# Kernel optimization log

Measured on AMD Instinct MI355X. Metric: run time of the kernel, lower is better.

Reference implementation:

```python
import jax, jax.numpy as jnp
import numpy as np

H = 1024          # hidden_size
RH = 2 * H        # router/expert hidden (hidden_multiplier=2)
E = 3             # num_experts
B, T, P = 8, 2048, 64
LN_EPS = 1e-5


def _layer_norm(x, gamma, beta):
    mu = jnp.mean(x, axis=-1, keepdims=True)
    var = jnp.mean(jnp.square(x - mu), axis=-1, keepdims=True)
    return (x - mu) * jax.lax.rsqrt(var + LN_EPS) * gamma + beta


def setup_inputs() -> dict:
    key = jax.random.key(0)
    ks = jax.random.split(key, 24)
    s = lambda fan_in: 1.0 / np.sqrt(fan_in)
    inp = {
        "mix_hidden_states": jax.random.normal(ks[0], (B, T, H), jnp.float32),
        "global_anchor": jax.random.normal(ks[1], (B, H), jnp.float32),
        "prototype_bank": jax.random.normal(ks[2], (B, P, H), jnp.float32),
        # LayerNorm
        "ln_gamma": jnp.ones((H,), jnp.float32),
        "ln_beta": jnp.zeros((H,), jnp.float32),
        # retriever (no bias)
        "Wq": jax.random.normal(ks[3], (H, H), jnp.float32) * s(H),
        "Wk": jax.random.normal(ks[4], (H, H), jnp.float32) * s(H),
        "Wv": jax.random.normal(ks[5], (H, H), jnp.float32) * s(H),
        # router linear: 3H -> E
        "router_W": jax.random.normal(ks[6], (3 * H, E), jnp.float32) * s(3 * H),
        "router_b": jnp.zeros((E,), jnp.float32),
        # experts stacked: [E, 3H, RH] and [E, RH, H]
        "e_w1": jax.random.normal(ks[7], (E, 3 * H, RH), jnp.float32) * s(3 * H),
        "e_b1": jnp.zeros((E, RH), jnp.float32),
        "e_w2": jax.random.normal(ks[8], (E, RH, H), jnp.float32) * s(RH),
        "e_b2": jnp.zeros((E, H), jnp.float32),
        # gate MLP: 3H -> H -> H
        "gate_w1": jax.random.normal(ks[9], (3 * H, H), jnp.float32) * s(3 * H),
        "gate_b1": jnp.zeros((H,), jnp.float32),
        "gate_w2": jax.random.normal(ks[10], (H, H), jnp.float32) * s(H),
        "gate_b2": jnp.zeros((H,), jnp.float32),
        # out_proj (zero-init in torch, but use random for nontrivial baseline)
        "out_w": jax.random.normal(ks[11], (H, H), jnp.float32) * s(H),
        "out_b": jnp.zeros((H,), jnp.float32),
    }
    return inp


def reference(mix_hidden_states, global_anchor, prototype_bank,
              ln_gamma, ln_beta, Wq, Wk, Wv, router_W, router_b,
              e_w1, e_b1, e_w2, e_b2, gate_w1, gate_b1, gate_w2, gate_b2,
              out_w, out_b):
    x = mix_hidden_states
    nx = _layer_norm(x, ln_gamma, ln_beta)                      # [B,T,H]

    # --- evidence retriever (cross-attention over prototype bank) ---
    q = nx @ Wq                                                 # [B,T,H]
    k = prototype_bank @ Wk                                     # [B,P,H]
    v = prototype_bank @ Wv                                     # [B,P,H]
    scores = jnp.einsum('bth,bph->btp', q, k) * (H ** -0.5)
    weights = jax.nn.softmax(scores, axis=-1)
    evidence = jnp.einsum('btp,bph->bth', weights, v)           # [B,T,H]

    anchor = jnp.broadcast_to(global_anchor[:, None, :], nx.shape)
    combined = jnp.concatenate([nx, evidence, anchor], axis=-1) # [B,T,3H]

    # --- soft MoE router ---
    router_logits = combined @ router_W + router_b              # [B,T,E]
    router_probs = jax.nn.softmax(router_logits, axis=-1)
    h = jax.nn.silu(jnp.einsum('btc,ecr->bter', combined, e_w1) + e_b1)
    expert_out = jnp.einsum('bter,erh->bteh', h, e_w2) + e_b2   # [B,T,E,H]
    routed = jnp.sum(expert_out * router_probs[..., None], axis=-2)

    # --- sigmoid gate + residual ---
    g = jax.nn.sigmoid(jax.nn.silu(combined @ gate_w1 + gate_b1) @ gate_w2 + gate_b2)
    refined_delta = g * (routed @ out_w + out_b)
    return x + refined_delta
```

## Files before the change

### kernel.cpp

```cpp
#include <hip/hip_runtime.h>

typedef unsigned short u16;
typedef __bf16 bf16x8 __attribute__((ext_vector_type(8)));
typedef float f32x4 __attribute__((ext_vector_type(4)));

__device__ __forceinline__ float b2f(u16 u) {
  union { unsigned int i; float f; } x; x.i = ((unsigned int)u) << 16; return x.f;
}
__device__ __forceinline__ u16 f2b(float f) {
  union { float f; unsigned int i; } x; x.f = f;
  unsigned int r = (x.i + 0x7fffu + ((x.i >> 16) & 1u)) >> 16;
  return (u16)r;
}

__device__ __forceinline__ void async16(const void* g, void* l) {
  __builtin_amdgcn_global_load_lds((const __attribute__((address_space(1))) void*)g,
                                   (__attribute__((address_space(3))) void*)l, 16, 0, 0);
}

#define EPI_BF16    0
#define EPI_SILU    1
#define EPI_SIGMOID 2
#define EPI_ROUTED  3
#define EPI_FINAL   4
#define EPI_F32SC   5

__global__ __launch_bounds__(256) void gemm_bt(
    const u16* __restrict__ A, int lda, long long sA,
    const u16* __restrict__ B, int ldb, long long sB,
    const float* __restrict__ bias,
    const float* __restrict__ bcast, int ldbc,
    void* __restrict__ Cv, int ldc, long long sC,
    int M, int N, int K,
    int epi, float scale,
    const float* __restrict__ rowscale, int rs_off, int accum,
    const float* __restrict__ Xres, const u16* __restrict__ Gg)
{
  __shared__ u16 As[2][128 * 32];
  __shared__ u16 Bs[2][128 * 32];
  const int z = blockIdx.z;
  A += (long long)z * sA;
  B += (long long)z * sB;
  const int m0 = blockIdx.y * 128, n0 = blockIdx.x * 128;
  const int tid = threadIdx.x;
  const int lane = tid & 63, w = tid >> 6;
  const int wm = w >> 1, wn = w & 1;

  const int sr = lane >> 2;
  const int sc = (lane & 3) * 8;
  int ra0 = m0 + w * 16 + sr;      if (ra0 > M - 1) ra0 = M - 1;
  int ra1 = m0 + 64 + w * 16 + sr; if (ra1 > M - 1) ra1 = M - 1;
  int rb0 = n0 + w * 16 + sr;      if (rb0 > N - 1) rb0 = N - 1;
  int rb1 = n0 + 64 + w * 16 + sr; if (rb1 > N - 1) rb1 = N - 1;
  const u16* pa0 = A + (long long)ra0 * lda + sc;
  const u16* pa1 = A + (long long)ra1 * lda + sc;
  const u16* pb0 = B + (long long)rb0 * ldb + sc;
  const u16* pb1 = B + (long long)rb1 * ldb + sc;
  const int lw = w * 512;

  f32x4 acc[4][4] = {};

  const int kch = (lane >> 4) * 8;
  const int rr = lane & 15;

  async16(pa0, &As[0][lw]);
  async16(pa1, &As[0][2048 + lw]);
  async16(pb0, &Bs[0][lw]);
  async16(pb1, &Bs[0][2048 + lw]);

  int cur = 0;
  for (int k0 = 0; k0 < K; k0 += 32) {
    __syncthreads();
    const int kn = k0 + 32;
    if (kn < K) {
      const int nb = cur ^ 1;
      async16(pa0 + kn, &As[nb][lw]);
      async16(pa1 + kn, &As[nb][2048 + lw]);
      async16(pb0 + kn, &Bs[nb][lw]);
      async16(pb1 + kn, &Bs[nb][2048 + lw]);
    }
    bf16x8 af[4], bfr[4];
#pragma unroll
    for (int mi = 0; mi < 4; ++mi)
      af[mi] = *(const bf16x8*)(&As[cur][(wm * 64 + mi * 16 + rr) * 32 + kch]);
#pragma unroll
    for (int ni = 0; ni < 4; ++ni)
      bfr[ni] = *(const bf16x8*)(&Bs[cur][(wn * 64 + ni * 16 + rr) * 32 + kch]);
#pragma unroll
    for (int mi = 0; mi < 4; ++mi)
#pragma unroll
      for (int ni = 0; ni < 4; ++ni)
        acc[mi][ni] = __builtin_amdgcn_mfma_f32_16x16x32_bf16(af[mi], bfr[ni], acc[mi][ni], 0, 0, 0);
    cur ^= 1;
  }

  u16* Cb = (u16*)Cv;
  float* Cf = (float*)Cv;
#pragma unroll
  for (int ni = 0; ni < 4; ++ni) {
    int col = n0 + wn * 64 + ni * 16 + (lane & 15);
    if (col >= N) continue;
    float bv = bias ? bias[col] : 0.0f;
#pragma unroll
    for (int mi = 0; mi < 4; ++mi) {
#pragma unroll
      for (int r = 0; r < 4; ++r) {
        int row = m0 + wm * 64 + mi * 16 + (lane >> 4) * 4 + r;
        if (row >= M) continue;
        float v = acc[mi][ni][r] + bv;
        if (bcast) v += bcast[(row >> 11) * ldbc + col];
        long long cidx = (long long)z * sC + (long long)row * ldc + col;
        if (epi == EPI_BF16) {
          Cb[cidx] = f2b(v);
        } else if (epi == EPI_SILU) {
          Cb[cidx] = f2b(v / (1.0f + __expf(-v)));
        } else if (epi == EPI_SIGMOID) {
          Cb[cidx] = f2b(1.0f / (1.0f + __expf(-v)));
        } else if (epi == EPI_ROUTED) {
          float rs = rowscale[row * 3 + rs_off];
          if (accum) Cf[cidx] += rs * v; else Cf[cidx] = rs * v;
        } else if (epi == EPI_FINAL) {
          long long xi = (long long)row * ldc + col;
          Cf[cidx] = Xres[xi] + b2f(Gg[xi]) * v;
        } else {
          Cf[cidx] = v * scale;
        }
      }
    }
  }
}

#define CFENCE asm volatile("" ::: "memory")

#define STAGE(H, T_, SLOT) do { \
  const u16* s_ = ((H) & 1) ? srcB : srcA; \
  const long long ld_ = ((H) & 1) ? (long long)ldb : (long long)lda; \
  const u16* p_ = s_ + (((H) >> 1) ? 128 * ld_ : 0) + (long long)(T_) * 64; \
  u16* lb_ = &lds8[SLOT][w * 1024]; \
  async16(p_, lb_); \
  async16(p_ + 8 * ld_, lb_ + 512); \
} while (0)

#define READA(SLOT) do { \
  _Pragma("unroll") for (int fm = 0; fm < 4; ++fm) { \
    af[fm][0] = *(const bf16x8*)&lds8[SLOT][(wm * 64 + fm * 16 + rr) * 64 + cx0]; \
    af[fm][1] = *(const bf16x8*)&lds8[SLOT][(wm * 64 + fm * 16 + rr) * 64 + cx1]; \
  } } while (0)

#define READB(SLOT) do { \
  _Pragma("unroll") for (int fn = 0; fn < 2; ++fn) { \
    bf[fn][0] = *(const bf16x8*)&lds8[SLOT][(wn * 32 + fn * 16 + rr) * 64 + cx0]; \
    bf[fn][1] = *(const bf16x8*)&lds8[SLOT][(wn * 32 + fn * 16 + rr) * 64 + cx1]; \
  } } while (0)

#define MMAC(QM, QN) do { \
  __builtin_amdgcn_s_setprio(1); \
  _Pragma("unroll") for (int fm = 0; fm < 4; ++fm) { \
    _Pragma("unroll") for (int fn = 0; fn < 2; ++fn) { \
      acc[(QM)*4+fm][(QN)*2+fn] = __builtin_amdgcn_mfma_f32_16x16x32_bf16(af[fm][0], bf[fn][0], acc[(QM)*4+fm][(QN)*2+fn], 0, 0, 0); \
      acc[(QM)*4+fm][(QN)*2+fn] = __builtin_amdgcn_mfma_f32_16x16x32_bf16(af[fm][1], bf[fn][1], acc[(QM)*4+fm][(QN)*2+fn], 0, 0, 0); \
    } } \
  __builtin_amdgcn_s_setprio(0); \
} while (0)

__global__ __launch_bounds__(512, 2) void gemm256_bt(
    const u16* __restrict__ A, int lda,
    const u16* __restrict__ B, int ldb,
    const float* __restrict__ bias,
    const float* __restrict__ bcast, int ldbc,
    void* __restrict__ Cv, int ldc,
    int M, int N, int K,
    int epi, float scale,
    const float* __restrict__ rowscale, int rs_off, int accum,
    const float* __restrict__ Xres, const u16* __restrict__ Gg)
{
  __shared__ u16 lds8[8][8192];

  int gx = gridDim.x;
  int nwg = gx * gridDim.y;
  int bid = blockIdx.y * gx + blockIdx.x;
  int bx, by;
  if ((nwg & 7) == 0) {
    int cpx = nwg >> 3;
    int swz = (bid & 7) * cpx + (bid >> 3);
    bx = swz % gx; by = swz / gx;
  } else { bx = blockIdx.x; by = blockIdx.y; }
  const int m0 = by * 256, n0 = bx * 256;

  const int tid = threadIdx.x;
  const int lane = tid & 63, w = tid >> 6;
  const int wm = w >> 2, wn = w & 3;
  const int rr = lane & 15;

  const int cx0 = (((lane >> 4) * 16)      ^ ((lane & 7) << 4)) >> 1;
  const int cx1 = ((64 + (lane >> 4) * 16) ^ ((lane & 7) << 4)) >> 1;

  const int rloc = w * 16 + (lane >> 3);
  const int swz8 = 8 * ((lane & 7) ^ (lane >> 3));
  const u16* srcA = A + (long long)(m0 + rloc) * lda + swz8;
  const u16* srcB = B + (long long)(n0 + rloc) * ldb + swz8;

  f32x4 acc[8][4] = {};
  bf16x8 af[4][2], bf[2][2];

  const int T = K >> 6;

  STAGE(0, 0, 0); STAGE(1, 0, 1); STAGE(2, 0, 2); STAGE(3, 0, 3);
  if (T > 1) { STAGE(0, 1, 4); STAGE(1, 1, 5); }
  if (T > 1) { asm volatile("s_waitcnt vmcnt(4)" ::: "memory"); }
  else       { asm volatile("s_waitcnt vmcnt(0)" ::: "memory"); }
  __builtin_amdgcn_s_barrier();
  CFENCE;

  for (int s = 0; s < T; ++s) {
    const int par = (s & 1) * 4;
    const int opar = 4 - par;

    READA(par + 0);
    READB(par + 1);
    CFENCE;
    if (s + 1 < T) STAGE(2, s + 1, opar + 2);
    __builtin_amdgcn_s_barrier();
    CFENCE;
    MMAC(0, 0);
    __builtin_amdgcn_s_barrier();
    CFENCE;

    READB(par + 3);
    CFENCE;
    if (s + 1 < T) STAGE(3, s + 1, opar + 3);
    __builtin_amdgcn_s_barrier();
    CFENCE;
    MMAC(0, 1);
    __builtin_amdgcn_s_barrier();
    CFENCE;

    READA(par + 2);
    READB(par + 1);
    CFENCE;
    if (s + 2 < T) STAGE(0, s + 2, par + 0);
    __builtin_amdgcn_s_barrier();
    CFENCE;
    MMAC(1, 0);
    __builtin_amdgcn_s_barrier();
    CFENCE;

    READB(par + 3);
    CFENCE;
    if (s + 2 < T) {
      STAGE(1, s + 2, par + 1);
      asm volatile("s_waitcnt vmcnt(4)" ::: "memory");
    } else if (s + 1 < T) {
      asm volatile("s_waitcnt vmcnt(0)" ::: "memory");
    }
    __builtin_amdgcn_s_barrier();
    CFENCE;
    MMAC(1, 1);
    __builtin_amdgcn_s_barrier();
    CFENCE;
  }

  u16* Cb = (u16*)Cv;
  float* Cf = (float*)Cv;
#pragma unroll
  for (int ni = 0; ni < 4; ++ni) {
    int col = n0 + (ni >> 1) * 128 + wn * 32 + (ni & 1) * 16 + (lane & 15);
    float bv = bias ? bias[col] : 0.0f;
#pragma unroll
    for (int mi = 0; mi < 8; ++mi) {
#pragma unroll
      for (int r = 0; r < 4; ++r) {
        int row = m0 + (mi >> 2) * 128 + wm * 64 + (mi & 3) * 16 + (lane >> 4) * 4 + r;
        float v = acc[mi][ni][r] + bv;
        if (bcast) v += bcast[(row >> 11) * ldbc + col];
        long long cidx = (long long)row * ldc + col;
        if (epi == EPI_BF16) {
          Cb[cidx] = f2b(v);
        } else if (epi == EPI_SILU) {
          Cb[cidx] = f2b(v / (1.0f + __expf(-v)));
        } else if (epi == EPI_SIGMOID) {
          Cb[cidx] = f2b(1.0f / (1.0f + __expf(-v)));
        } else if (epi == EPI_ROUTED) {
          float rs = rowscale[row * 3 + rs_off];
          if (accum) Cf[cidx] += rs * v; else Cf[cidx] = rs * v;
        } else if (epi == EPI_FINAL) {
          long long xi = (long long)row * ldc + col;
          Cf[cidx] = Xres[xi] + b2f(Gg[xi]) * v;
        } else {
          Cf[cidx] = v * scale;
        }
      }
    }
  }
}

__global__ __launch_bounds__(256) void transpose_cvt(const float* __restrict__ in, u16* __restrict__ out, int R, int C) {
  __shared__ float tile[32][33];
  int c0 = blockIdx.x * 32, r0 = blockIdx.y * 32;
  int tx = threadIdx.x & 31, ty = threadIdx.x >> 5;
#pragma unroll
  for (int i = 0; i < 4; ++i) {
    int r = ty + i * 8;
    tile[r][tx] = in[(long long)(r0 + r) * C + c0 + tx];
  }
  __syncthreads();
#pragma unroll
  for (int i = 0; i < 4; ++i) {
    int r = ty + i * 8;
    out[(long long)(c0 + r) * R + r0 + tx] = f2b(tile[tx][r]);
  }
}

__global__ __launch_bounds__(256) void cvt_bf16(const float* __restrict__ in, u16* __restrict__ out, int n) {
  for (int i = blockIdx.x * 256 + threadIdx.x; i < n; i += gridDim.x * 256)
    out[i] = f2b(in[i]);
}

__global__ __launch_bounds__(256) void ln_kernel(const float* __restrict__ x, const float* __restrict__ gamma,
                                                 const float* __restrict__ beta, u16* __restrict__ ne) {
  int t = blockIdx.x;
  int tid = threadIdx.x;
  const float* xr = x + (long long)t * 1024;
  float v[4];
  float s = 0.f, sq = 0.f;
#pragma unroll
  for (int i = 0; i < 4; ++i) {
    v[i] = xr[tid * 4 + i];
    s += v[i]; sq += v[i] * v[i];
  }
#pragma unroll
  for (int d = 32; d; d >>= 1) { s += __shfl_xor(s, d, 64); sq += __shfl_xor(sq, d, 64); }
  __shared__ float ls[4], lq[4];
  int w = tid >> 6, lane = tid & 63;
  if (lane == 0) { ls[w] = s; lq[w] = sq; }
  __syncthreads();
  s = ls[0] + ls[1] + ls[2] + ls[3];
  sq = lq[0] + lq[1] + lq[2] + lq[3];
  float mean = s * (1.0f / 1024.0f);
  float var = sq * (1.0f / 1024.0f) - mean * mean;
  float rstd = rsqrtf(var + 1e-5f);
  long long base = (long long)t * 2048;
#pragma unroll
  for (int i = 0; i < 4; ++i) {
    int c = tid * 4 + i;
    ne[base + c] = f2b((v[i] - mean) * rstd * gamma[c] + beta[c]);
  }
}

#define ANCH_KC 32
__global__ __launch_bounds__(256) void anchor_partial(const float* __restrict__ anchor, const float* __restrict__ W,
                                                      int ldw, int N, float* __restrict__ partial) {
  int n = blockIdx.x * 256 + threadIdx.x;
  if (n >= N) return;
  const int kc = blockIdx.y;
  const int kper = 1024 / ANCH_KC;
  const int k0 = kc * kper;
  float acc[8] = {};
  for (int k = k0; k < k0 + kper; ++k) {
    float wv = W[(long long)(2048 + k) * ldw + n];
#pragma unroll
    for (int b = 0; b < 8; ++b) acc[b] += anchor[b * 1024 + k] * wv;
  }
#pragma unroll
  for (int b = 0; b < 8; ++b)
    partial[((long long)kc * 8 + b) * N + n] = acc[b];
}

__global__ __launch_bounds__(256) void anchor_reduce(const float* __restrict__ partial, int N, float* __restrict__ bc) {
  int i = blockIdx.x * 256 + threadIdx.x;
  if (i >= 8 * N) return;
  float s = 0.f;
#pragma unroll 8
  for (int kc = 0; kc < ANCH_KC; ++kc) s += partial[(long long)kc * 8 * N + i];
  bc[i] = s;
}

__global__ __launch_bounds__(256) void attn_softmax(const float* __restrict__ scores, u16* __restrict__ weights) {
  int gid = blockIdx.x * 256 + threadIdx.x;
  int t = gid >> 6, lane = gid & 63;
  float sv = scores[(long long)t * 64 + lane];
  float m = sv;
#pragma unroll
  for (int d = 32; d; d >>= 1) m = fmaxf(m, __shfl_xor(m, d, 64));
  float e = __expf(sv - m);
  float sum = e;
#pragma unroll
  for (int d = 32; d; d >>= 1) sum += __shfl_xor(sum, d, 64);
  weights[(long long)t * 64 + lane] = f2b(e / sum);
}

__global__ __launch_bounds__(256) void router_kernel(const u16* __restrict__ ne, const float* __restrict__ anchor,
                                                     const float* __restrict__ rW, const float* __restrict__ rb,
                                                     float* __restrict__ probs) {
  int gid = blockIdx.x * 256 + threadIdx.x;
  int t = gid >> 6, lane = gid & 63;
  int b = t >> 11;
  const u16* cr = ne + (long long)t * 2048;
  const float* ar = anchor + (long long)b * 1024;
  float s0 = 0.f, s1 = 0.f, s2 = 0.f;
  for (int c = lane; c < 2048; c += 64) {
    float xv = b2f(cr[c]);
    s0 += xv * rW[c * 3 + 0];
    s1 += xv * rW[c * 3 + 1];
    s2 += xv * rW[c * 3 + 2];
  }
  for (int c = lane; c < 1024; c += 64) {
    float xv = ar[c];
    s0 += xv * rW[(2048 + c) * 3 + 0];
    s1 += xv * rW[(2048 + c) * 3 + 1];
    s2 += xv * rW[(2048 + c) * 3 + 2];
  }
#pragma unroll
  for (int d = 32; d; d >>= 1) {
    s0 += __shfl_xor(s0, d, 64);
    s1 += __shfl_xor(s1, d, 64);
    s2 += __shfl_xor(s2, d, 64);
  }
  s0 += rb[0]; s1 += rb[1]; s2 += rb[2];
  float m = fmaxf(s0, fmaxf(s1, s2));
  float e0 = __expf(s0 - m), e1 = __expf(s1 - m), e2 = __expf(s2 - m);
  float inv = 1.0f / (e0 + e1 + e2);
  if (lane == 0) {
    probs[(long long)t * 3 + 0] = e0 * inv;
    probs[(long long)t * 3 + 1] = e1 * inv;
    probs[(long long)t * 3 + 2] = e2 * inv;
  }
}

extern "C" void kernel_launch(void* const* d_in, const int* in_sizes, int n_in,
                              void* d_out, int out_size, void* d_ws, size_t ws_size,
                              hipStream_t stream) {
  const float* X      = (const float*)d_in[0];
  const float* anchor = (const float*)d_in[1];
  const float* proto  = (const float*)d_in[2];
  const float* gamma  = (const float*)d_in[3];
  const float* beta   = (const float*)d_in[4];
  const float* Wq     = (const float*)d_in[5];
  const float* Wk     = (const float*)d_in[6];
  const float* Wv     = (const float*)d_in[7];
  const float* rW     = (const float*)d_in[8];
  const float* rb     = (const float*)d_in[9];
  const float* ew1    = (const float*)d_in[10];
  const float* eb1    = (const float*)d_in[11];
  const float* ew2    = (const float*)d_in[12];
  const float* eb2    = (const float*)d_in[13];
  const float* gw1    = (const float*)d_in[14];
  const float* gb1    = (const float*)d_in[15];
  const float* gw2    = (const float*)d_in[16];
  const float* gb2    = (const float*)d_in[17];
  const float* ow     = (const float*)d_in[18];
  const float* ob     = (const float*)d_in[19];
  float* out = (float*)d_out;

  char* p = (char*)d_ws;
  size_t used = 0;
  auto alloc = [&](size_t bytes) {
    char* r = p; size_t a = (bytes + 255) & ~((size_t)255);
    p += a; used += a; return r;
  };
  u16* ne     = (u16*)alloc(16384ull * 2048 * 2);
  u16* S1     = (u16*)alloc(16384ull * 2048 * 2);
  float* routed = (float*)alloc(16384ull * 1024 * 4);
  u16* w8     = (u16*)alloc(2048ull * 2048 * 2);
  u16* proto_bf = (u16*)alloc(512ull * 1024 * 2);
  u16* kbuf   = (u16*)alloc(512ull * 1024 * 2);
  u16* v_t    = (u16*)alloc(1024ull * 512 * 2);
  u16* wts    = (u16*)alloc(16384ull * 64 * 2);
  float* scores = (float*)alloc(16384ull * 64 * 4);
  float* probs  = (float*)alloc(16384ull * 3 * 4);
  float* anch   = (float*)alloc(8ull * 2048 * 4);
  float* anchp  = (float*)alloc((size_t)ANCH_KC * 8 * 2048 * 4);
  if (used > ws_size) return;

  u16* gh = S1;
  u16* g  = S1 + 16384ull * 1024;
  u16* routed_bf = S1;

  auto gemm = [&](const u16* A, int lda, long long sA,
                  const u16* B, int ldb, long long sB,
                  const float* bias, const float* bcast, int ldbc,
                  void* C, int ldc, long long sC,
                  int M, int N, int K, int Z,
                  int epi, float scale, const float* rs, int rs_off, int accum,
                  const float* Xr, const u16* Gg) {
    bool big = (Z == 1) && (M % 256 == 0) && (N % 256 == 0) && (K % 64 == 0) && (K >= 128) && (M >= 2048);
    if (big) {
      dim3 grd(N / 256, M / 256, 1);
      gemm256_bt<<<grd, 512, 0, stream>>>(A, lda, B, ldb, bias, bcast, ldbc,
                                          C, ldc, M, N, K, epi, scale, rs, rs_off, accum, Xr, Gg);
    } else {
      dim3 grd((N + 127) / 128, (M + 127) / 128, Z);
      gemm_bt<<<grd, 256, 0, stream>>>(A, lda, sA, B, ldb, sB, bias, bcast, ldbc,
                                       C, ldc, sC, M, N, K, epi, scale, rs, rs_off, accum, Xr, Gg);
    }
  };

  auto anchor_term = [&](const float* W, int ldw, int N, float* bc) {
    anchor_partial<<<dim3((N + 255) / 256, ANCH_KC), 256, 0, stream>>>(anchor, W, ldw, N, anchp);
    anchor_reduce<<<(8 * N + 255) / 256, 256, 0, stream>>>(anchp, N, bc);
  };

  ln_kernel<<<16384, 256, 0, stream>>>(X, gamma, beta, ne);
  cvt_bf16<<<512, 256, 0, stream>>>(proto, proto_bf, 512 * 1024);

  transpose_cvt<<<dim3(32, 32), 256, 0, stream>>>(Wk, w8, 1024, 1024);
  gemm(proto_bf, 1024, 0, w8, 1024, 0, nullptr, nullptr, 0, kbuf, 1024, 0,
       512, 1024, 1024, 1, EPI_BF16, 0.f, nullptr, 0, 0, nullptr, nullptr);

  transpose_cvt<<<dim3(32, 32), 256, 0, stream>>>(Wv, w8, 1024, 1024);
  gemm(w8, 1024, 0, proto_bf, 1024, 0, nullptr, nullptr, 0, v_t, 512, 0,
       1024, 512, 1024, 1, EPI_BF16, 0.f, nullptr, 0, 0, nullptr, nullptr);

  transpose_cvt<<<dim3(32, 32), 256, 0, stream>>>(Wq, w8, 1024, 1024);
  gemm(ne, 2048, 0, w8, 1024, 0, nullptr, nullptr, 0, S1, 1024, 0,
       16384, 1024, 1024, 1, EPI_BF16, 0.f, nullptr, 0, 0, nullptr, nullptr);

  gemm(S1, 1024, 2048ll * 1024, kbuf, 1024, 64ll * 1024, nullptr, nullptr, 0,
       scores, 64, 2048ll * 64, 2048, 64, 1024, 8, EPI_F32SC, 0.03125f, nullptr, 0, 0, nullptr, nullptr);
  attn_softmax<<<4096, 256, 0, stream>>>(scores, wts);
  gemm(wts, 64, 2048ll * 64, v_t, 512, 64, nullptr, nullptr, 0,
       ne + 1024, 2048, 2048ll * 2048, 2048, 1024, 64, 8, EPI_BF16, 0.f, nullptr, 0, 0, nullptr, nullptr);

  router_kernel<<<4096, 256, 0, stream>>>(ne, anchor, rW, rb, probs);

  for (int e = 0; e < 3; ++e) {
    const float* W1 = ew1 + (long long)e * 3072 * 2048;
    const float* W2 = ew2 + (long long)e * 2048 * 1024;
    transpose_cvt<<<dim3(64, 64), 256, 0, stream>>>(W1, w8, 2048, 2048);
    anchor_term(W1, 2048, 2048, anch);
    gemm(ne, 2048, 0, w8, 2048, 0, eb1 + e * 2048, anch, 2048, S1, 2048, 0,
         16384, 2048, 2048, 1, EPI_SILU, 0.f, nullptr, 0, 0, nullptr, nullptr);
    transpose_cvt<<<dim3(32, 64), 256, 0, stream>>>(W2, w8, 2048, 1024);
    gemm(S1, 2048, 0, w8, 2048, 0, eb2 + e * 1024, nullptr, 0, routed, 1024, 0,
         16384, 1024, 2048, 1, EPI_ROUTED, 0.f, probs, e, (e > 0) ? 1 : 0, nullptr, nullptr);
  }

  transpose_cvt<<<dim3(32, 64), 256, 0, stream>>>(gw1, w8, 2048, 1024);
  anchor_term(gw1, 1024, 1024, anch);
  gemm(ne, 2048, 0, w8, 2048, 0, gb1, anch, 1024, gh, 1024, 0,
       16384, 1024, 2048, 1, EPI_SILU, 0.f, nullptr, 0, 0, nullptr, nullptr);
  transpose_cvt<<<dim3(32, 32), 256, 0, stream>>>(gw2, w8, 1024, 1024);
  gemm(gh, 1024, 0, w8, 1024, 0, gb2, nullptr, 0, g, 1024, 0,
       16384, 1024, 1024, 1, EPI_SIGMOID, 0.f, nullptr, 0, 0, nullptr, nullptr);

  cvt_bf16<<<4096, 256, 0, stream>>>(routed, routed_bf, 16777216);
  transpose_cvt<<<dim3(32, 32), 256, 0, stream>>>(ow, w8, 1024, 1024);
  gemm(routed_bf, 1024, 0, w8, 1024, 0, ob, nullptr, 0, out, 1024, 0,
       16384, 1024, 1024, 1, EPI_FINAL, 0.f, nullptr, 0, 0, X, g);
}
```

Baseline: 2.291 ms.

## Keep both A and B fragments in registers and prefetch two k-steps ahead

The GEMM main loop now holds separate register fragment sets (a0/a1, b0/b1), so each LDS half-tile is read once per k-step instead of re-reading B halves. The global-to-LDS prefetch schedule changes so that all four sub-tiles of step s+2 are issued during step s, with a deeper vmcnt wait. The aim is to cut LDS read traffic and hide global load latency better, at the cost of more vector registers under a launch bound of 2 blocks per CU.

```diff
diff --git a/kernel.cpp b/kernel.cpp
--- a/kernel.cpp
+++ b/kernel.cpp
@@ -141,24 +141,24 @@
   async16(p_ + 8 * ld_, lb_ + 512); \
 } while (0)
 
-#define READA(SLOT) do { \
+#define READA(SLOT, DST) do { \
   _Pragma("unroll") for (int fm = 0; fm < 4; ++fm) { \
-    af[fm][0] = *(const bf16x8*)&lds8[SLOT][(wm * 64 + fm * 16 + rr) * 64 + cx0]; \
-    af[fm][1] = *(const bf16x8*)&lds8[SLOT][(wm * 64 + fm * 16 + rr) * 64 + cx1]; \
+    DST[fm][0] = *(const bf16x8*)&lds8[SLOT][(wm * 64 + fm * 16 + rr) * 64 + cx0]; \
+    DST[fm][1] = *(const bf16x8*)&lds8[SLOT][(wm * 64 + fm * 16 + rr) * 64 + cx1]; \
   } } while (0)
 
-#define READB(SLOT) do { \
+#define READB(SLOT, DST) do { \
   _Pragma("unroll") for (int fn = 0; fn < 2; ++fn) { \
-    bf[fn][0] = *(const bf16x8*)&lds8[SLOT][(wn * 32 + fn * 16 + rr) * 64 + cx0]; \
-    bf[fn][1] = *(const bf16x8*)&lds8[SLOT][(wn * 32 + fn * 16 + rr) * 64 + cx1]; \
+    DST[fn][0] = *(const bf16x8*)&lds8[SLOT][(wn * 32 + fn * 16 + rr) * 64 + cx0]; \
+    DST[fn][1] = *(const bf16x8*)&lds8[SLOT][(wn * 32 + fn * 16 + rr) * 64 + cx1]; \
   } } while (0)
 
-#define MMAC(QM, QN) do { \
+#define MMAC(QM, QN, AF, BF) do { \
   __builtin_amdgcn_s_setprio(1); \
   _Pragma("unroll") for (int fm = 0; fm < 4; ++fm) { \
     _Pragma("unroll") for (int fn = 0; fn < 2; ++fn) { \
-      acc[(QM)*4+fm][(QN)*2+fn] = __builtin_amdgcn_mfma_f32_16x16x32_bf16(af[fm][0], bf[fn][0], acc[(QM)*4+fm][(QN)*2+fn], 0, 0, 0); \
-      acc[(QM)*4+fm][(QN)*2+fn] = __builtin_amdgcn_mfma_f32_16x16x32_bf16(af[fm][1], bf[fn][1], acc[(QM)*4+fm][(QN)*2+fn], 0, 0, 0); \
+      acc[(QM)*4+fm][(QN)*2+fn] = __builtin_amdgcn_mfma_f32_16x16x32_bf16(AF[fm][0], BF[fn][0], acc[(QM)*4+fm][(QN)*2+fn], 0, 0, 0); \
+      acc[(QM)*4+fm][(QN)*2+fn] = __builtin_amdgcn_mfma_f32_16x16x32_bf16(AF[fm][1], BF[fn][1], acc[(QM)*4+fm][(QN)*2+fn], 0, 0, 0); \
     } } \
   __builtin_amdgcn_s_setprio(0); \
 } while (0)
@@ -201,61 +201,58 @@
   const u16* srcB = B + (long long)(n0 + rloc) * ldb + swz8;
 
   f32x4 acc[8][4] = {};
-  bf16x8 af[4][2], bf[2][2];
+  bf16x8 a0[4][2], a1[4][2], b0[2][2], b1[2][2];
 
   const int T = K >> 6;
 
   STAGE(0, 0, 0); STAGE(1, 0, 1); STAGE(2, 0, 2); STAGE(3, 0, 3);
-  if (T > 1) { STAGE(0, 1, 4); STAGE(1, 1, 5); }
-  if (T > 1) { asm volatile("s_waitcnt vmcnt(4)" ::: "memory"); }
-  else       { asm volatile("s_waitcnt vmcnt(0)" ::: "memory"); }
+  if (T > 1) {
+    STAGE(0, 1, 4); STAGE(1, 1, 5); STAGE(2, 1, 6); STAGE(3, 1, 7);
+    asm volatile("s_waitcnt vmcnt(8)" ::: "memory");
+  } else {
+    asm volatile("s_waitcnt vmcnt(0)" ::: "memory");
+  }
   __builtin_amdgcn_s_barrier();
   CFENCE;
 
   for (int s = 0; s < T; ++s) {
     const int par = (s & 1) * 4;
-    const int opar = 4 - par;
-
-    READA(par + 0);
-    READB(par + 1);
-    CFENCE;
-    if (s + 1 < T) STAGE(2, s + 1, opar + 2);
-    __builtin_amdgcn_s_barrier();
-    CFENCE;
-    MMAC(0, 0);
-    __builtin_amdgcn_s_barrier();
-    CFENCE;
-
-    READB(par + 3);
-    CFENCE;
-    if (s + 1 < T) STAGE(3, s + 1, opar + 3);
-    __builtin_amdgcn_s_barrier();
-    CFENCE;
-    MMAC(0, 1);
-    __builtin_amdgcn_s_barrier();
-    CFENCE;
-
-    READA(par + 2);
-    READB(par + 1);
-    CFENCE;
-    if (s + 2 < T) STAGE(0, s + 2, par + 0);
-    __builtin_amdgcn_s_barrier();
-    CFENCE;
-    MMAC(1, 0);
-    __builtin_amdgcn_s_barrier();
-    CFENCE;
-
-    READB(par + 3);
-    CFENCE;
-    if (s + 2 < T) {
-      STAGE(1, s + 2, par + 1);
-      asm volatile("s_waitcnt vmcnt(4)" ::: "memory");
-    } else if (s + 1 < T) {
-      asm volatile("s_waitcnt vmcnt(0)" ::: "memory");
-    }
-    __builtin_amdgcn_s_barrier();
-    CFENCE;
-    MMAC(1, 1);
+    const bool pf = (s + 2 < T);
+
+    READA(par + 0, a0);
+    READB(par + 1, b0);
+    CFENCE;
+    __builtin_amdgcn_s_barrier();
+    CFENCE;
+    MMAC(0, 0, a0, b0);
+    __builtin_amdgcn_s_barrier();
+    CFENCE;
+
+    READB(par + 3, b1);
+    CFENCE;
+    if (pf) { STAGE(0, s + 2, par + 0); STAGE(1, s + 2, par + 1); }
+    __builtin_amdgcn_s_barrier();
+    CFENCE;
+    MMAC(0, 1, a0, b1);
+    __builtin_amdgcn_s_barrier();
+    CFENCE;
+
+    READA(par + 2, a1);
+    CFENCE;
+    if (pf) STAGE(3, s + 2, par + 3);
+    __builtin_amdgcn_s_barrier();
+    CFENCE;
+    MMAC(1, 0, a1, b0);
+    __builtin_amdgcn_s_barrier();
+    CFENCE;
+
+    if (pf) STAGE(2, s + 2, par + 2);
+    CFENCE;
+    __builtin_amdgcn_s_barrier();
+    CFENCE;
+    MMAC(1, 1, a1, b1);
+    if (pf)                 asm volatile("s_waitcnt vmcnt(8)" ::: "memory");
+    else if (s + 1 < T)     asm volatile("s_waitcnt vmcnt(0)" ::: "memory");
     __builtin_amdgcn_s_barrier();
     CFENCE;
   }
```

Measured after the change: 2.307 ms. Within noise of the previous version (+0.7%).
